# Kernel optimization log

Hardware: AMD Instinct MI355X
Metric: run time of the kernel (lower is better)

## Reference

```python
import jax, jax.numpy as jnp
import numpy as np
import math

B, S, C, H = 32, 500, 1024, 16
D = C // H  # head dim = 64

def setup_inputs() -> dict:
    key = jax.random.key(0)
    ks = jax.random.split(key, 9)
    sc = 1.0 / math.sqrt(C)
    return {
        "x": jax.random.normal(ks[0], (B, S, C), dtype=jnp.float32),
        "Wq": jax.random.normal(ks[1], (C, C), dtype=jnp.float32) * sc,
        "bq": jnp.zeros((C,), dtype=jnp.float32),
        "Wk": jax.random.normal(ks[2], (C, C), dtype=jnp.float32) * sc,
        "bk": jnp.zeros((C,), dtype=jnp.float32),
        "Wv": jax.random.normal(ks[3], (C, C), dtype=jnp.float32) * sc,
        "bv": jnp.zeros((C,), dtype=jnp.float32),
        "Wp": jax.random.normal(ks[4], (C, C), dtype=jnp.float32) * sc,
        "bp": jnp.zeros((C,), dtype=jnp.float32),
    }

def reference(x, Wq, bq, Wk, bk, Wv, bv, Wp, bp):
    # Projections -> [B, H, S, D]
    q = (x @ Wq + bq).reshape(B, S, H, D).transpose(0, 2, 1, 3)
    k = (x @ Wk + bk).reshape(B, S, H, D).transpose(0, 2, 1, 3)
    v = (x @ Wv + bv).reshape(B, S, H, D).transpose(0, 2, 1, 3)
    # Scaled scores [B, H, S, S]
    att = jnp.einsum('bhqd,bhkd->bhqk', q, k) * (1.0 / math.sqrt(D))
    causal = jnp.tril(jnp.ones((S, S), dtype=bool))
    att = jnp.where(causal[None, None], att, jnp.float32(-1e10))
    att = jax.nn.softmax(att, axis=-1)
    # (dropout is identity in eval mode)
    y = jnp.einsum('bhqk,bhkd->bhqd', att, v)  # [B, H, S, D]
    y = y.transpose(0, 2, 1, 3).reshape(B, S, C)
    return y @ Wp + bp
```

## Files before the change

### kernel.cpp

```cpp
#include <hip/hip_runtime.h>
#include <math.h>

#define B_ 32
#define S_ 500
#define C_ 1024
#define H_ 16
#define D_ 64
#define M_ (B_ * S_)
#define SP 512

typedef _Float16 f16;
typedef f16 f16x8 __attribute__((ext_vector_type(8)));
typedef f16 f16x4 __attribute__((ext_vector_type(4)));
typedef float f32x4 __attribute__((ext_vector_type(4)));

#define GLOBAL_AS __attribute__((address_space(1)))
#define LDS_AS __attribute__((address_space(3)))

__device__ __forceinline__ void async_load16(const void* g, void* l) {
    __builtin_amdgcn_global_load_lds((const GLOBAL_AS void*)g, (LDS_AS void*)l, 16, 0, 0);
}

struct MaskF { static constexpr bool value = false; };
struct MaskT { static constexpr bool value = true; };

__global__ __launch_bounds__(256) void cast_rows(
    const float* __restrict__ in, f16* __restrict__ out, int n8)
{
    int i = blockIdx.x * 256 + threadIdx.x;
    if (i >= n8) return;
    float4 a = ((const float4*)in)[2 * i];
    float4 b = ((const float4*)in)[2 * i + 1];
    f16x8 h;
    h[0] = (f16)a.x; h[1] = (f16)a.y; h[2] = (f16)a.z; h[3] = (f16)a.w;
    h[4] = (f16)b.x; h[5] = (f16)b.y; h[6] = (f16)b.z; h[7] = (f16)b.w;
    ((f16x8*)out)[i] = h;
}

__global__ __launch_bounds__(256) void castW_T(
    const float* __restrict__ W, f16* __restrict__ T)
{
    __shared__ float t[32][33];
    const int n0 = blockIdx.x * 32, k0 = blockIdx.y * 32;
    const int tx = threadIdx.x, ty = threadIdx.y;
#pragma unroll
    for (int i = 0; i < 4; ++i)
        t[ty + 8 * i][tx] = W[(size_t)(k0 + ty + 8 * i) * C_ + n0 + tx];
    __syncthreads();
#pragma unroll
    for (int i = 0; i < 4; ++i) {
        int n = ty + 8 * i;
        T[(size_t)(n0 + n) * C_ + k0 + tx] = (f16)t[tx][n];
    }
}

template <int MODE>
__global__ __launch_bounds__(256) void gemm_mfma(
    const f16* __restrict__ A, const f16* __restrict__ W,
    const float* __restrict__ b0, const float* __restrict__ b1,
    const float* __restrict__ b2, void* __restrict__ o0,
    void* __restrict__ o1, void* __restrict__ o2)
{
    constexpr int K = C_;
    constexpr int NB = (MODE == 0) ? 24 : 8;
    constexpr int CHUNK = (NB * 125) / 8;
    __shared__ __align__(16) f16 sA[128 * 32];
    __shared__ __align__(16) f16 sW[128 * 32];

    const int tid = threadIdx.x;
    const int lin = blockIdx.x;
    const int bid = (lin & 7) * CHUNK + (lin >> 3);
    const int m0 = (bid / NB) * 128;
    const int n0 = (bid % NB) * 128;
    const int lane = tid & 63;
    const int w = tid >> 6;
    const int wm = (w & 1) * 64;
    const int wn = (w >> 1) * 64;
    const int quad = lane >> 4;
    const int lr = lane & 15;

    const f16* gA[2];
    const f16* gW[2];
    f16* lA[2];
    f16* lW[2];
#pragma unroll
    for (int p = 0; p < 2; ++p) {
        int slot = p * 256 + tid;
        int row = slot >> 2, c = slot & 3;
        int csw = c ^ ((row >> 1) & 3);
        gA[p] = A + (size_t)(m0 + row) * K + csw * 8;
        gW[p] = W + (size_t)(n0 + row) * K + csw * 8;
        lA[p] = &sA[slot * 8];
        lW[p] = &sW[slot * 8];
    }

    f32x4 acc[4][4];
#pragma unroll
    for (int i = 0; i < 4; ++i)
#pragma unroll
        for (int j = 0; j < 4; ++j) acc[i][j] = (f32x4)0.f;

    int offA[4], offB[4];
#pragma unroll
    for (int t = 0; t < 4; ++t) {
        int m = wm + t * 16 + lr;
        offA[t] = m * 32 + (quad ^ ((m >> 1) & 3)) * 8;
        int n = wn + t * 16 + lr;
        offB[t] = n * 32 + (quad ^ ((n >> 1) & 3)) * 8;
    }

    for (int k0 = 0; k0 < K; k0 += 32) {
#pragma unroll
        for (int p = 0; p < 2; ++p) {
            async_load16(gA[p] + k0, lA[p]);
            async_load16(gW[p] + k0, lW[p]);
        }
        __syncthreads();

        f16x8 af[4], bf[4];
#pragma unroll
        for (int t = 0; t < 4; ++t) {
            af[t] = *(const f16x8*)&sA[offA[t]];
            bf[t] = *(const f16x8*)&sW[offB[t]];
        }
#pragma unroll
        for (int mt = 0; mt < 4; ++mt)
#pragma unroll
            for (int nt = 0; nt < 4; ++nt)
                acc[mt][nt] = __builtin_amdgcn_mfma_f32_16x16x32_f16(
                    af[mt], bf[nt], acc[mt][nt], 0, 0, 0);
        __syncthreads();
    }

#pragma unroll
    for (int nt = 0; nt < 4; ++nt) {
        int gc = n0 + wn + nt * 16 + lr;
        if (MODE == 1) {
            float bv = b0[gc];
            float* of = (float*)o0;
#pragma unroll
            for (int mt = 0; mt < 4; ++mt) {
                int gr0 = m0 + wm + mt * 16 + quad * 4;
#pragma unroll
                for (int r = 0; r < 4; ++r)
                    of[(size_t)(gr0 + r) * C_ + gc] = acc[mt][nt][r] + bv;
            }
        } else {
            int sec = gc >> 10;
            int gcl = gc & 1023;
            const float* bp = (sec == 0) ? b0 : (sec == 1) ? b1 : b2;
            float bv = bp[gcl];
            float osc = (sec == 0) ? 0.125f : 1.0f;
            int h = gcl >> 6, d = gcl & 63;
#pragma unroll
            for (int mt = 0; mt < 4; ++mt) {
                int gr0 = m0 + wm + mt * 16 + quad * 4;
                int b = gr0 / S_, s0 = gr0 - b * S_;
                if (sec < 2) {
                    f16* oq = (f16*)((sec == 0) ? o0 : o1);
#pragma unroll
                    for (int r = 0; r < 4; ++r) {
                        float v = (acc[mt][nt][r] + bv) * osc;
                        size_t idx = (((size_t)b * H_ + h) * S_ + (s0 + r)) * D_ + d;
                        oq[idx] = (f16)v;
                    }
                } else {
                    f16* ov = (f16*)o2;
                    f16x4 pk;
#pragma unroll
                    for (int r = 0; r < 4; ++r) pk[r] = (f16)(acc[mt][nt][r] + bv);
                    *(f16x4*)(ov + (((size_t)b * H_ + h) * D_ + d) * SP + s0) = pk;
                }
            }
        }
    }
}

__global__ __launch_bounds__(256) void attn_mfma(
    const f16* __restrict__ qg, const f16* __restrict__ kg,
    const f16* __restrict__ vt, f16* __restrict__ Y)
{
    __shared__ __align__(16) f16 sK[2][64 * 64];
    __shared__ __align__(16) f16 sVt[2][64 * 64];
    __shared__ __align__(16) f16 sP[4 * 32 * 64];

    const int tid = threadIdx.x;
    const int lin = blockIdx.x;
    const int xcd = lin & 7;
    const int pos = lin >> 3;
    const int bh = xcd * 64 + (pos >> 2);
    const int qt = 3 - (pos & 3);
    const int q0 = qt * 128;
    const int lane = tid & 63, w = tid >> 6;
    const int quad = lane >> 4, lr = lane & 15;
    const size_t gbase = (size_t)bh * S_ * D_;
    const size_t vbase = (size_t)bh * D_ * SP;
    const int psw = (lr & 7) << 1;

    f16x8 qf[2][2];
#pragma unroll
    for (int t = 0; t < 2; ++t) {
        int q = q0 + w * 32 + t * 16 + lr;
        const f16* pq = qg + gbase + (size_t)q * D_;
#pragma unroll
        for (int s2 = 0; s2 < 2; ++s2)
            qf[t][s2] = *(const f16x8*)(pq + quad * 8 + 32 * s2);
    }

    f32x4 accO[2][4];
#pragma unroll
    for (int t = 0; t < 2; ++t)
#pragma unroll
        for (int nt = 0; nt < 4; ++nt) accO[t][nt] = (f32x4)0.f;
    float l_run[2] = {0.f, 0.f};

    const int NT = 2 * qt + 2;

    auto stage = [&](int kt, int buf) __attribute__((always_inline)) {
        const int k0 = kt * 64;
#pragma unroll
        for (int it = 0; it < 2; ++it) {
            int idx = it * 256 + tid;
            int row = idx >> 3, c = idx & 7;
            int csw = (c ^ (row & 7)) * 8;
            async_load16(kg + gbase + (size_t)(k0 + row) * D_ + csw, &sK[buf][idx * 8]);
            async_load16(vt + vbase + (size_t)row * SP + k0 + csw, &sVt[buf][idx * 8]);
        }
    };

    auto step = [&](int kt, auto masked_tag) __attribute__((always_inline)) {
        constexpr bool MASKED = decltype(masked_tag)::value;
        const int cur = kt & 1;
        if (kt + 1 < NT) stage(kt + 1, cur ^ 1);
        const int k0 = kt * 64;

        f32x4 accS[4][2];
#pragma unroll
        for (int mt = 0; mt < 4; ++mt)
#pragma unroll
            for (int t = 0; t < 2; ++t) accS[mt][t] = (f32x4)0.f;
#pragma unroll
        for (int mt = 0; mt < 4; ++mt) {
            int row = mt * 16 + lr;
#pragma unroll
            for (int s2 = 0; s2 < 2; ++s2) {
                int off = row * 64 + (((quad + 4 * s2) ^ (lr & 7)) << 3);
                f16x8 ka = *(const f16x8*)&sK[cur][off];
#pragma unroll
                for (int t = 0; t < 2; ++t)
                    accS[mt][t] = __builtin_amdgcn_mfma_f32_16x16x32_f16(
                        ka, qf[t][s2], accS[mt][t], 0, 0, 0);
            }
        }

        float ls[2] = {0.f, 0.f};
#pragma unroll
        for (int mt = 0; mt < 4; ++mt)
#pragma unroll
            for (int t = 0; t < 2; ++t) {
                f16x4 pk;
#pragma unroll
                for (int r = 0; r < 4; ++r) {
                    float s = accS[mt][t][r];
                    if (MASKED) {
                        int key = k0 + mt * 16 + quad * 4 + r;
                        int qq = q0 + w * 32 + t * 16 + lr;
                        s = (key <= qq && key < S_) ? s : -1e30f;
                    }
                    float p = __expf(s);
                    ls[t] += p;
                    pk[r] = (f16)p;
                }
                int c8 = (mt * 4 + quad) ^ psw;
                *(f16x4*)&sP[w * 2048 + (t * 16 + lr) * 64 + c8 * 4] = pk;
            }
        ls[0] += __shfl_xor(ls[0], 16); ls[0] += __shfl_xor(ls[0], 32);
        ls[1] += __shfl_xor(ls[1], 16); ls[1] += __shfl_xor(ls[1], 32);
        l_run[0] += ls[0];
        l_run[1] += ls[1];

#pragma unroll
        for (int t = 0; t < 2; ++t) {
            int pb = w * 2048 + (t * 16 + lr) * 64;
#pragma unroll
            for (int s2 = 0; s2 < 2; ++s2) {
                int c8 = (quad * 2 + 8 * s2) ^ psw;
                f16x8 pf = *(const f16x8*)&sP[pb + c8 * 4];
#pragma unroll
                for (int nt = 0; nt < 4; ++nt) {
                    f16x8 vf = *(const f16x8*)
                        &sVt[cur][(nt * 16 + lr) * 64 + (((quad + 4 * s2) ^ (lr & 7)) << 3)];
                    accO[t][nt] = __builtin_amdgcn_mfma_f32_16x16x32_f16(
                        pf, vf, accO[t][nt], 0, 0, 0);
                }
            }
        }
        __syncthreads();
    };

    stage(0, 0);
    __syncthreads();
    for (int kt = 0; kt < 2 * qt; ++kt) step(kt, MaskF{});
    step(2 * qt, MaskT{});
    step(2 * qt + 1, MaskT{});

    const int b = bh >> 4, h = bh & 15;
#pragma unroll
    for (int t = 0; t < 2; ++t) {
#pragma unroll
        for (int r = 0; r < 4; ++r) {
            float lsum = __shfl(l_run[t], quad * 4 + r);
            float iv = 1.f / lsum;
            int s = q0 + w * 32 + t * 16 + quad * 4 + r;
            if (s >= S_) continue;
            size_t rowbase = (size_t)(b * S_ + s) * C_ + h * 64;
#pragma unroll
            for (int nt = 0; nt < 4; ++nt)
                Y[rowbase + nt * 16 + lr] = (f16)(accO[t][nt][r] * iv);
        }
    }
}

extern "C" void kernel_launch(void* const* d_in, const int* in_sizes, int n_in,
                              void* d_out, int out_size, void* d_ws, size_t ws_size,
                              hipStream_t stream)
{
    const float* x = (const float*)d_in[0];
    const float* Wq = (const float*)d_in[1];
    const float* bq = (const float*)d_in[2];
    const float* Wk = (const float*)d_in[3];
    const float* bk = (const float*)d_in[4];
    const float* Wv = (const float*)d_in[5];
    const float* bv = (const float*)d_in[6];
    const float* Wp = (const float*)d_in[7];
    const float* bp = (const float*)d_in[8];

    const size_t NEL = (size_t)M_ * C_;
    const size_t WEL = (size_t)C_ * C_;
    f16* qf = (f16*)d_ws;
    f16* kf = qf + NEL;
    f16* vtw = kf + NEL;
    f16* xf = vtw + (size_t)B_ * H_ * D_ * SP;
    f16* wpf = xf + NEL;
    f16* yf = xf;

    f16* wq = (f16*)d_out;
    f16* wk = wq + WEL;
    f16* wv = wk + WEL;

    dim3 tg(32, 32), tb(32, 8);
    castW_T<<<tg, tb, 0, stream>>>(Wq, wq);
    castW_T<<<tg, tb, 0, stream>>>(Wk, wk);
    castW_T<<<tg, tb, 0, stream>>>(Wv, wv);
    castW_T<<<tg, tb, 0, stream>>>(Wp, wpf);

    int n8 = (int)(NEL / 8);
    cast_rows<<<(n8 + 255) / 256, 256, 0, stream>>>(x, xf, n8);

    gemm_mfma<0><<<3000, 256, 0, stream>>>(xf, wq, bq, bk, bv, qf, kf, vtw);

    attn_mfma<<<2048, 256, 0, stream>>>(qf, kf, vtw, yf);

    gemm_mfma<1><<<1000, 256, 0, stream>>>(yf, wpf, bp, nullptr, nullptr,
                                           d_out, nullptr, nullptr);
}
```

Measured before the change: 393.6 us.

## Replace 128x128 GEMMs with double-buffered 256x256 tile MFMA kernel

Rewrites the projection GEMMs to use 256x256 output tiles per 512-thread workgroup, with a 64-wide K step. Global-to-LDS async loads are double-buffered and tracked with explicit vmcnt waits, MFMA phases are interleaved with fragment loads, and s_setprio raises priority during the MFMA phases. To fit the larger tile, the activation rows are padded to 16128 and zero-filled in the cast kernel, and the four weight cast/transpose launches are merged into one. The aim is more data reuse per LDS byte and better overlap of loads with compute. The cost is 128KB of dynamic LDS per block, which allows only one block per CU, along with heavier register pressure and a coarser tail across the grid.

```diff
diff --git a/kernel.cpp b/kernel.cpp
--- a/kernel.cpp
+++ b/kernel.cpp
@@ -7,6 +7,7 @@
 #define H_ 16
 #define D_ 64
 #define M_ (B_ * S_)
+#define MP 16128
 #define SP 512
 
 typedef _Float16 f16;
@@ -20,27 +21,43 @@
 __device__ __forceinline__ void async_load16(const void* g, void* l) {
     __builtin_amdgcn_global_load_lds((const GLOBAL_AS void*)g, (LDS_AS void*)l, 16, 0, 0);
 }
+template <int N>
+__device__ __forceinline__ void wait_vmcnt() {
+    asm volatile("s_waitcnt vmcnt(%0)" ::"i"(N) : "memory");
+}
 
 struct MaskF { static constexpr bool value = false; };
 struct MaskT { static constexpr bool value = true; };
 
 __global__ __launch_bounds__(256) void cast_rows(
-    const float* __restrict__ in, f16* __restrict__ out, int n8)
+    const float* __restrict__ in, f16* __restrict__ out, int n8_real, int n8_tot)
 {
     int i = blockIdx.x * 256 + threadIdx.x;
-    if (i >= n8) return;
-    float4 a = ((const float4*)in)[2 * i];
-    float4 b = ((const float4*)in)[2 * i + 1];
+    if (i >= n8_tot) return;
     f16x8 h;
-    h[0] = (f16)a.x; h[1] = (f16)a.y; h[2] = (f16)a.z; h[3] = (f16)a.w;
-    h[4] = (f16)b.x; h[5] = (f16)b.y; h[6] = (f16)b.z; h[7] = (f16)b.w;
+    if (i < n8_real) {
+        float4 a = ((const float4*)in)[2 * i];
+        float4 b = ((const float4*)in)[2 * i + 1];
+        h[0] = (f16)a.x; h[1] = (f16)a.y; h[2] = (f16)a.z; h[3] = (f16)a.w;
+        h[4] = (f16)b.x; h[5] = (f16)b.y; h[6] = (f16)b.z; h[7] = (f16)b.w;
+    } else {
+        f16 z = (f16)0.f;
+        h[0] = z; h[1] = z; h[2] = z; h[3] = z;
+        h[4] = z; h[5] = z; h[6] = z; h[7] = z;
+    }
     ((f16x8*)out)[i] = h;
 }
 
-__global__ __launch_bounds__(256) void castW_T(
-    const float* __restrict__ W, f16* __restrict__ T)
+__global__ __launch_bounds__(256) void castW_T4(
+    const float* __restrict__ W0, const float* __restrict__ W1,
+    const float* __restrict__ W2, const float* __restrict__ W3,
+    f16* __restrict__ T0, f16* __restrict__ T1,
+    f16* __restrict__ T2, f16* __restrict__ T3)
 {
     __shared__ float t[32][33];
+    const int z = blockIdx.z;
+    const float* W = (z == 0) ? W0 : (z == 1) ? W1 : (z == 2) ? W2 : W3;
+    f16* T = (z == 0) ? T0 : (z == 1) ? T1 : (z == 2) ? T2 : T3;
     const int n0 = blockIdx.x * 32, k0 = blockIdx.y * 32;
     const int tx = threadIdx.x, ty = threadIdx.y;
 #pragma unroll
@@ -54,113 +71,144 @@
     }
 }
 
+#define BAR()                          \
+    __builtin_amdgcn_s_barrier();      \
+    __builtin_amdgcn_sched_barrier(0)
+
+#define LD_A(MH)                                                              \
+    _Pragma("unroll") for (int i = 0; i < 4; ++i)                             \
+    _Pragma("unroll") for (int ks = 0; ks < 2; ++ks)                          \
+        af[i][ks] = *(const f16x8*)(smem + c * 32768 + rowA +                 \
+                                    ((MH) * 64 + i * 16) * 64 + sw[ks]);
+
+#define LD_B(NH)                                                              \
+    _Pragma("unroll") for (int j = 0; j < 2; ++j)                             \
+    _Pragma("unroll") for (int ks = 0; ks < 2; ++ks)                          \
+        bf[NH][j][ks] = *(const f16x8*)(smem + c * 32768 + rowB +             \
+                                        ((NH) * 32 + j * 16) * 64 + sw[ks]);
+
+#define MMA(MH, NH)                                                           \
+    __builtin_amdgcn_s_setprio(1);                                            \
+    _Pragma("unroll") for (int i = 0; i < 4; ++i)                             \
+    _Pragma("unroll") for (int j = 0; j < 2; ++j)                             \
+    _Pragma("unroll") for (int ks = 0; ks < 2; ++ks)                          \
+        acc[(MH) * 4 + i][(NH) * 2 + j] =                                     \
+            __builtin_amdgcn_mfma_f32_16x16x32_f16(                           \
+                af[i][ks], bf[NH][j][ks], acc[(MH) * 4 + i][(NH) * 2 + j],    \
+                0, 0, 0);                                                     \
+    __builtin_amdgcn_s_setprio(0)
+
 template <int MODE>
-__global__ __launch_bounds__(256) void gemm_mfma(
+__global__ __launch_bounds__(512) void gemm256(
     const f16* __restrict__ A, const f16* __restrict__ W,
     const float* __restrict__ b0, const float* __restrict__ b1,
     const float* __restrict__ b2, void* __restrict__ o0,
     void* __restrict__ o1, void* __restrict__ o2)
 {
     constexpr int K = C_;
-    constexpr int NB = (MODE == 0) ? 24 : 8;
-    constexpr int CHUNK = (NB * 125) / 8;
-    __shared__ __align__(16) f16 sA[128 * 32];
-    __shared__ __align__(16) f16 sW[128 * 32];
+    constexpr int NB = (MODE == 0) ? 12 : 4;
+    constexpr int NWG = 63 * NB;
+    constexpr int Q8 = NWG / 8, R8 = NWG % 8;
+    extern __shared__ __align__(16) f16 smem[];
 
     const int tid = threadIdx.x;
+    const int lane = tid & 63, w = tid >> 6;
+    const int wm = w >> 2, wn = w & 3;
+    const int quad = lane >> 4, lr = lane & 15;
+
     const int lin = blockIdx.x;
-    const int bid = (lin & 7) * CHUNK + (lin >> 3);
-    const int m0 = (bid / NB) * 128;
-    const int n0 = (bid % NB) * 128;
-    const int lane = tid & 63;
-    const int w = tid >> 6;
-    const int wm = (w & 1) * 64;
-    const int wn = (w >> 1) * 64;
-    const int quad = lane >> 4;
-    const int lr = lane & 15;
-
-    const f16* gA[2];
-    const f16* gW[2];
-    f16* lA[2];
-    f16* lW[2];
-#pragma unroll
-    for (int p = 0; p < 2; ++p) {
-        int slot = p * 256 + tid;
-        int row = slot >> 2, c = slot & 3;
-        int csw = c ^ ((row >> 1) & 3);
-        gA[p] = A + (size_t)(m0 + row) * K + csw * 8;
-        gW[p] = W + (size_t)(n0 + row) * K + csw * 8;
-        lA[p] = &sA[slot * 8];
-        lW[p] = &sW[slot * 8];
-    }
-
-    f32x4 acc[4][4];
-#pragma unroll
-    for (int i = 0; i < 4; ++i)
+    const int xcd = lin & 7, pos = lin >> 3;
+    const int wg = (xcd < R8 ? xcd * (Q8 + 1) : R8 * (Q8 + 1) + (xcd - R8) * Q8) + pos;
+    const int m0 = (wg / NB) * 256;
+    const int n0 = (wg % NB) * 256;
+
+    const int srow = tid >> 3, sj = tid & 7;
+    const int gc = sj ^ (srow & 7);
+    const f16* pA = A + (size_t)(m0 + srow) * K + gc * 8;
+    const f16* pB = W + (size_t)(n0 + srow) * K + gc * 8;
+    f16* dA = smem + tid * 8;
+    f16* dB = smem + 16384 + tid * 8;
+
+    auto stageA = [&](int kt, int cb, int h) __attribute__((always_inline)) {
+        const f16* s = pA + (size_t)(h * 128) * K + kt * 64;
+        f16* d = dA + cb * 32768 + h * 8192;
+        async_load16(s, d);
+        async_load16(s + (size_t)64 * K, d + 4096);
+    };
+    auto stageB = [&](int kt, int cb, int h) __attribute__((always_inline)) {
+        const f16* s = pB + (size_t)(h * 128) * K + kt * 64;
+        f16* d = dB + cb * 32768 + h * 8192;
+        async_load16(s, d);
+        async_load16(s + (size_t)64 * K, d + 4096);
+    };
+
+    int sw[2];
+    sw[0] = ((0 + quad) ^ (lr & 7)) * 8;
+    sw[1] = ((4 + quad) ^ (lr & 7)) * 8;
+    const int rowA = (wm * 128 + lr) * 64;
+    const int rowB = 16384 + (wn * 64 + lr) * 64;
+
+    f32x4 acc[8][4];
+#pragma unroll
+    for (int i = 0; i < 8; ++i)
 #pragma unroll
         for (int j = 0; j < 4; ++j) acc[i][j] = (f32x4)0.f;
-
-    int offA[4], offB[4];
-#pragma unroll
-    for (int t = 0; t < 4; ++t) {
-        int m = wm + t * 16 + lr;
-        offA[t] = m * 32 + (quad ^ ((m >> 1) & 3)) * 8;
-        int n = wn + t * 16 + lr;
-        offB[t] = n * 32 + (quad ^ ((n >> 1) & 3)) * 8;
-    }
-
-    for (int k0 = 0; k0 < K; k0 += 32) {
-#pragma unroll
-        for (int p = 0; p < 2; ++p) {
-            async_load16(gA[p] + k0, lA[p]);
-            async_load16(gW[p] + k0, lW[p]);
-        }
-        __syncthreads();
-
-        f16x8 af[4], bf[4];
-#pragma unroll
-        for (int t = 0; t < 4; ++t) {
-            af[t] = *(const f16x8*)&sA[offA[t]];
-            bf[t] = *(const f16x8*)&sW[offB[t]];
-        }
-#pragma unroll
-        for (int mt = 0; mt < 4; ++mt)
-#pragma unroll
-            for (int nt = 0; nt < 4; ++nt)
-                acc[mt][nt] = __builtin_amdgcn_mfma_f32_16x16x32_f16(
-                    af[mt], bf[nt], acc[mt][nt], 0, 0, 0);
-        __syncthreads();
-    }
-
-#pragma unroll
-    for (int nt = 0; nt < 4; ++nt) {
-        int gc = n0 + wn + nt * 16 + lr;
+    f16x8 af[4][2], bf[2][2][2];
+
+    stageA(0, 0, 0); stageA(0, 0, 1); stageB(0, 0, 0); stageB(0, 0, 1);
+
+    constexpr int NT = K / 64;
+    for (int kt = 0; kt < NT; ++kt) {
+        const int c = kt & 1;
+        BAR();
+        if (kt + 1 < NT) {
+            stageA(kt + 1, c ^ 1, 0); stageA(kt + 1, c ^ 1, 1);
+            stageB(kt + 1, c ^ 1, 0); stageB(kt + 1, c ^ 1, 1);
+            wait_vmcnt<8>();
+        } else {
+            wait_vmcnt<0>();
+        }
+        BAR();
+        LD_A(0); LD_B(0);
+        MMA(0, 0);
+        LD_B(1);
+        MMA(0, 1);
+        LD_A(1);
+        MMA(1, 1);
+        MMA(1, 0);
+    }
+
+#pragma unroll
+    for (int nf = 0; nf < 4; ++nf) {
+        int gcn = n0 + wn * 64 + nf * 16 + lr;
         if (MODE == 1) {
-            float bv = b0[gc];
+            float bv = b0[gcn];
             float* of = (float*)o0;
 #pragma unroll
-            for (int mt = 0; mt < 4; ++mt) {
-                int gr0 = m0 + wm + mt * 16 + quad * 4;
+            for (int mf = 0; mf < 8; ++mf) {
+                int gr0 = m0 + wm * 128 + mf * 16 + quad * 4;
+                if (gr0 >= M_) continue;
 #pragma unroll
                 for (int r = 0; r < 4; ++r)
-                    of[(size_t)(gr0 + r) * C_ + gc] = acc[mt][nt][r] + bv;
+                    of[(size_t)(gr0 + r) * C_ + gcn] = acc[mf][nf][r] + bv;
             }
         } else {
-            int sec = gc >> 10;
-            int gcl = gc & 1023;
+            int sec = gcn >> 10;
+            int gcl = gcn & 1023;
             const float* bp = (sec == 0) ? b0 : (sec == 1) ? b1 : b2;
             float bv = bp[gcl];
             float osc = (sec == 0) ? 0.125f : 1.0f;
             int h = gcl >> 6, d = gcl & 63;
 #pragma unroll
-            for (int mt = 0; mt < 4; ++mt) {
-                int gr0 = m0 + wm + mt * 16 + quad * 4;
+            for (int mf = 0; mf < 8; ++mf) {
+                int gr0 = m0 + wm * 128 + mf * 16 + quad * 4;
+                if (gr0 >= M_) continue;
                 int b = gr0 / S_, s0 = gr0 - b * S_;
                 if (sec < 2) {
                     f16* oq = (f16*)((sec == 0) ? o0 : o1);
 #pragma unroll
                     for (int r = 0; r < 4; ++r) {
-                        float v = (acc[mt][nt][r] + bv) * osc;
+                        float v = (acc[mf][nf][r] + bv) * osc;
                         size_t idx = (((size_t)b * H_ + h) * S_ + (s0 + r)) * D_ + d;
                         oq[idx] = (f16)v;
                     }
@@ -168,7 +216,7 @@
                     f16* ov = (f16*)o2;
                     f16x4 pk;
 #pragma unroll
-                    for (int r = 0; r < 4; ++r) pk[r] = (f16)(acc[mt][nt][r] + bv);
+                    for (int r = 0; r < 4; ++r) pk[r] = (f16)(acc[mf][nf][r] + bv);
                     *(f16x4*)(ov + (((size_t)b * H_ + h) * D_ + d) * SP + s0) = pk;
                 }
             }
@@ -341,26 +389,29 @@
     f16* kf = qf + NEL;
     f16* vtw = kf + NEL;
     f16* xf = vtw + (size_t)B_ * H_ * D_ * SP;
-    f16* wpf = xf + NEL;
+    f16* wpf = xf + (size_t)MP * C_;
     f16* yf = xf;
 
     f16* wq = (f16*)d_out;
     f16* wk = wq + WEL;
     f16* wv = wk + WEL;
 
-    dim3 tg(32, 32), tb(32, 8);
-    castW_T<<<tg, tb, 0, stream>>>(Wq, wq);
-    castW_T<<<tg, tb, 0, stream>>>(Wk, wk);
-    castW_T<<<tg, tb, 0, stream>>>(Wv, wv);
-    castW_T<<<tg, tb, 0, stream>>>(Wp, wpf);
-
-    int n8 = (int)(NEL / 8);
-    cast_rows<<<(n8 + 255) / 256, 256, 0, stream>>>(x, xf, n8);
-
-    gemm_mfma<0><<<3000, 256, 0, stream>>>(xf, wq, bq, bk, bv, qf, kf, vtw);
+    hipFuncSetAttribute(reinterpret_cast<const void*>(&gemm256<0>),
+                        hipFuncAttributeMaxDynamicSharedMemorySize, 131072);
+    hipFuncSetAttribute(reinterpret_cast<const void*>(&gemm256<1>),
+                        hipFuncAttributeMaxDynamicSharedMemorySize, 131072);
+
+    castW_T4<<<dim3(32, 32, 4), dim3(32, 8), 0, stream>>>(
+        Wq, Wk, Wv, Wp, wq, wk, wv, wpf);
+
+    int n8r = (int)(NEL / 8);
+    int n8t = (int)((size_t)MP * C_ / 8);
+    cast_rows<<<(n8t + 255) / 256, 256, 0, stream>>>(x, xf, n8r, n8t);
+
+    gemm256<0><<<756, 512, 131072, stream>>>(xf, wq, bq, bk, bv, qf, kf, vtw);
 
     attn_mfma<<<2048, 256, 0, stream>>>(qf, kf, vtw, yf);
 
-    gemm_mfma<1><<<1000, 256, 0, stream>>>(yf, wpf, bp, nullptr, nullptr,
-                                           d_out, nullptr, nullptr);
-}
+    gemm256<1><<<252, 512, 131072, stream>>>(yf, wpf, bp, nullptr, nullptr,
+                                             d_out, nullptr, nullptr);
+}
```

After: 375.7 us. 1.05x faster.
